# Kernel tuning notes

Measured on AMD Instinct MI355X. Metric: run time of the kernel, lower is better.

The kernel has to match this reference:

```python
import jax, jax.numpy as jnp
import numpy as np

B, N, F, T, O, K = 4, 4000, 16, 16, 16, 3
LN_EPS = 1e-5


def setup_inputs() -> dict:
    key = jax.random.key(0)
    k = jax.random.split(key, 18)
    rn = lambda i, sh, sc=1.0: jax.random.normal(k[i], sh, dtype=jnp.float32) * np.float32(sc)
    ru = lambda i, sh: jax.random.uniform(k[i], sh, dtype=jnp.float32)
    return {
        "x": rn(0, (B, N, F, T)),
        # scale the random Laplacian so the Chebyshev recurrence stays numerically sane
        "laplacian": rn(1, (N, N), 1.0 / np.sqrt(N)),
        "W1": ru(2, (T,)),
        "W2": rn(3, (F, T)),
        "W3": ru(4, (F,)),
        "bs": ru(5, (1, N, N)),
        "Vs": ru(6, (N, N)),
        "U1": ru(7, (N,)),
        "U2": rn(8, (F, N)),
        "U3": ru(9, (F,)),
        "be": ru(10, (1, T, T)),
        "Ve": ru(11, (T, T)),
        "cheb_w": rn(12, (K, F, O), 1.0 / np.sqrt(F)),
        "time_w": rn(13, (O, F, T), 1.0 / np.sqrt(F * T)),
        "time_b": rn(14, (O,)),
        "ln_g": jnp.ones((N, O), dtype=jnp.float32),
        "ln_b": jnp.zeros((N, O), dtype=jnp.float32),
    }


def reference(x, laplacian, W1, W2, W3, bs, Vs, U1, U2, U3, be, Ve,
              cheb_w, time_w, time_b, ln_g, ln_b):
    # ---- temporal attention: E (B,T,T) ----
    # lhs[b,t] = sum_{n,f} x[b,n,f,t] * U1[n]
    t_lhs = jnp.einsum('bnft,n->bt', x, U1)
    # rhs[b,t] = sum_{n,f,g} x[b,n,f,t] * U2[g,n] * U3[g]
    t_rhs = jnp.einsum('bnft,gn,g->bt', x, U2, U3)
    t_prod = t_lhs[:, :, None] * t_rhs[:, None, :]          # (B,T,T) outer product
    E = jnp.einsum('ts,bsr->btr', Ve, jax.nn.sigmoid(t_prod + be))
    E = jax.nn.softmax(E, axis=-1)

    # apply temporal attention along the time axis: (B,N,F,T)
    x_TAt = jnp.einsum('bts,bnfs->bnft', E, x)

    # ---- spatial attention: S (B,N,N) ----
    s_lhs = jnp.einsum('bnft,t->bnf', x, W1)                 # (B,N,F)
    # faithful to the source ops (valid since F == T here)
    s_rhs = jnp.einsum('bnkt,gk,t->bng', x, W2, W3)          # (B,N,F)
    s_prod = jnp.einsum('bnf,bmf->bnm', s_lhs, s_rhs)        # (B,N,N)
    S = jnp.einsum('nm,bmk->bnk', Vs, jax.nn.sigmoid(s_prod + bs))
    S = jax.nn.softmax(S, axis=-1)

    # spatially attended features for all timesteps at once
    x_SAtt = jnp.einsum('bnm,bmft->bnft', S, x_TAt)          # (B,N,F,T)

    # ---- Chebyshev graph conv over every timestep ----
    Tx0 = x_SAtt
    out = jnp.einsum('bnft,fo->bnot', Tx0, cheb_w[0])
    Tx1 = jnp.einsum('nm,bmft->bnft', laplacian, Tx0)
    out = out + jnp.einsum('bnft,fo->bnot', Tx1, cheb_w[1])
    for kk in range(2, K):
        Tx2 = 2.0 * jnp.einsum('nm,bmft->bnft', laplacian, Tx1) - Tx0
        out = out + jnp.einsum('bnft,fo->bnot', Tx2, cheb_w[kk])
        Tx0, Tx1 = Tx1, Tx2
    spatial_gcn_avg = out.mean(axis=-1)                      # (B,N,O)

    # ---- time conv: Conv2d(in,out,kernel=(1,T)) == full contraction over (F,T) ----
    time_out = jnp.einsum('bnct,oct->bno', x, time_w) + time_b

    # ---- residual (in_channels == out_channels branch) ----
    residual = x[:, :, :, -1]                                # (B,N,O)

    y = spatial_gcn_avg + time_out + residual
    # LayerNorm over the last two dims [N, O]
    mean = y.mean(axis=(1, 2), keepdims=True)
    var = jnp.var(y, axis=(1, 2), keepdims=True)
    y = (y - mean) / jnp.sqrt(var + LN_EPS) * ln_g + ln_b
    return jax.nn.relu(y)
```

## Files before the change

kernel.cpp:

```cpp
#include <hip/hip_runtime.h>
#include <math.h>

#define Bc 4
#define Nn 4000
#define KS 4096
#define NP (16000000 + 4096)

typedef _Float16 half8 __attribute__((ext_vector_type(8)));
typedef float f32x4 __attribute__((ext_vector_type(4)));
typedef unsigned short u16x4 __attribute__((ext_vector_type(4)));

static __device__ __forceinline__ unsigned short f2h(float f) {
  _Float16 h = (_Float16)f;
  unsigned short u;
  __builtin_memcpy(&u, &h, 2);
  return u;
}
static __device__ __forceinline__ float h2f(unsigned short u) {
  _Float16 h;
  __builtin_memcpy(&h, &u, 2);
  return (float)h;
}
static __device__ __forceinline__ void gld16(const void* g, void* l) {
  __builtin_amdgcn_global_load_lds(
      (const __attribute__((address_space(1))) unsigned int*)g,
      (__attribute__((address_space(3))) unsigned int*)l, 16, 0, 0);
}

__global__ __launch_bounds__(256) void k1_trhs(
    const float* __restrict__ x, const float* __restrict__ U1,
    const float* __restrict__ U2, const float* __restrict__ U3,
    float* __restrict__ tl, float* __restrict__ tr) {
  int b = blockIdx.y;
  int tid = threadIdx.x;
  int q = tid & 3;
  int n = blockIdx.x * 64 + (tid >> 2);
  float xs[16];
#pragma unroll
  for (int t = 0; t < 16; ++t) xs[t] = 0.f;
  float c1 = 0.f, c2 = 0.f;
  if (n < Nn) {
    const float* xr = x + ((size_t)b * Nn + n) * 256 + q * 64;
#pragma unroll
    for (int f = 0; f < 4; ++f) {
#pragma unroll
      for (int qq = 0; qq < 4; ++qq) {
        float4 v = *(const float4*)(xr + f * 16 + qq * 4);
        xs[qq * 4 + 0] += v.x; xs[qq * 4 + 1] += v.y;
        xs[qq * 4 + 2] += v.z; xs[qq * 4 + 3] += v.w;
      }
    }
    c1 = U1[n];
#pragma unroll
    for (int g = 0; g < 4; ++g) {
      int gg = q * 4 + g;
      c2 += U2[(size_t)gg * Nn + n] * U3[gg];
    }
  }
#pragma unroll
  for (int m = 1; m < 4; m <<= 1) {
    c2 += __shfl_xor(c2, m, 64);
#pragma unroll
    for (int t = 0; t < 16; ++t) xs[t] += __shfl_xor(xs[t], m, 64);
  }
  float v1[4], v2[4];
#pragma unroll
  for (int i = 0; i < 4; ++i) {
    int t = q * 4 + i;
    v1[i] = c1 * xs[t];
    v2[i] = c2 * xs[t];
  }
#pragma unroll
  for (int off = 4; off < 64; off <<= 1) {
#pragma unroll
    for (int i = 0; i < 4; ++i) {
      v1[i] += __shfl_down(v1[i], off, 64);
      v2[i] += __shfl_down(v2[i], off, 64);
    }
  }
  int lane = tid & 63;
  if (lane < 4) {
#pragma unroll
    for (int i = 0; i < 4; ++i) {
      atomicAdd(&tl[b * 16 + lane * 4 + i], v1[i]);
      atomicAdd(&tr[b * 16 + lane * 4 + i], v2[i]);
    }
  }
}

__global__ __launch_bounds__(256) void k2_eattn(
    const float* __restrict__ tl, const float* __restrict__ tr,
    const float* __restrict__ be, const float* __restrict__ Ve,
    float* __restrict__ ecol) {
  int b = blockIdx.x;
  int tid = threadIdx.x;
  __shared__ float sig[256];
  __shared__ float Em[256];
  int s = tid >> 4, r = tid & 15;
  float z = tl[b * 16 + s] * tr[b * 16 + r] + be[s * 16 + r];
  sig[s * 16 + r] = 1.0f / (1.0f + __expf(-z));
  __syncthreads();
  float e = 0.f;
#pragma unroll
  for (int ss = 0; ss < 16; ++ss) e += Ve[s * 16 + ss] * sig[ss * 16 + r];
  Em[s * 16 + r] = e;
  __syncthreads();
  if (tid < 16) {
    float m = -1e30f;
#pragma unroll
    for (int rr = 0; rr < 16; ++rr) m = fmaxf(m, Em[tid * 16 + rr]);
    float ssum = 0.f;
    float ex[16];
#pragma unroll
    for (int rr = 0; rr < 16; ++rr) { ex[rr] = __expf(Em[tid * 16 + rr] - m); ssum += ex[rr]; }
    float inv = 1.0f / ssum;
#pragma unroll
    for (int rr = 0; rr < 16; ++rr) Em[tid * 16 + rr] = ex[rr] * inv;
  }
  __syncthreads();
  if (tid < 16) {
    float c = 0.f;
#pragma unroll
    for (int tt = 0; tt < 16; ++tt) c += Em[tt * 16 + tid];
    ecol[b * 16 + tid] = c;
  }
}

__global__ __launch_bounds__(256) void k3_pern(
    const float* __restrict__ x, const float* __restrict__ ecol,
    const float* __restrict__ W1, const float* __restrict__ W2,
    const float* __restrict__ W3, const float* __restrict__ time_w,
    const float* __restrict__ time_b,
    float* __restrict__ xts, float* __restrict__ slhs,
    float* __restrict__ srhs, float* __restrict__ base) {
  __shared__ float tws[4096];
  __shared__ float W1s[16], W3s[16], Ecs[16], tbs[16], W2s[256];
  int tid = threadIdx.x;
  int b = blockIdx.y;
  for (int i = tid; i < 4096; i += 256) tws[i] = time_w[i];
  W2s[tid] = W2[tid & 255];
  if (tid < 16) {
    W1s[tid] = W1[tid]; W3s[tid] = W3[tid];
    Ecs[tid] = ecol[b * 16 + tid]; tbs[tid] = time_b[tid];
  }
  __syncthreads();
  int n = blockIdx.x * 256 + tid;
  if (n >= Nn) return;
  const float* xr = x + ((size_t)b * Nn + n) * 256;
  float xtsv[16], slv[16], xw3[16], to[16], resid[16];
#pragma unroll
  for (int i = 0; i < 16; ++i) { xtsv[i] = 0; slv[i] = 0; xw3[i] = 0; to[i] = 0; }
  for (int f = 0; f < 16; ++f) {
    float xf[16];
#pragma unroll
    for (int q = 0; q < 4; ++q) {
      float4 v = *(const float4*)(xr + f * 16 + q * 4);
      xf[q * 4 + 0] = v.x; xf[q * 4 + 1] = v.y; xf[q * 4 + 2] = v.z; xf[q * 4 + 3] = v.w;
    }
    float a = 0, c = 0, d = 0;
#pragma unroll
    for (int t2 = 0; t2 < 16; ++t2) {
      a += Ecs[t2] * xf[t2];
      c += W1s[t2] * xf[t2];
      d += W3s[t2] * xf[t2];
    }
    xtsv[f] = a; slv[f] = c; xw3[f] = d; resid[f] = xf[15];
#pragma unroll
    for (int o = 0; o < 16; ++o) {
      float acc = 0;
#pragma unroll
      for (int t2 = 0; t2 < 16; ++t2) acc += tws[o * 256 + f * 16 + t2] * xf[t2];
      to[o] += acc;
    }
  }
  size_t o16 = ((size_t)b * Nn + n) * 16;
#pragma unroll
  for (int g = 0; g < 16; ++g) {
    float acc = 0;
#pragma unroll
    for (int k2 = 0; k2 < 16; ++k2) acc += W2s[g * 16 + k2] * xw3[k2];
    srhs[o16 + g] = acc;
  }
#pragma unroll
  for (int i = 0; i < 16; ++i) {
    xts[o16 + i] = xtsv[i];
    slhs[o16 + i] = slv[i];
    base[o16 + i] = to[i] + tbs[i] + resid[i];
  }
}

__global__ __launch_bounds__(256) void fconv(
    const float* __restrict__ src, unsigned short* __restrict__ dst) {
  size_t i = ((size_t)blockIdx.x * 256 + threadIdx.x) * 4;
  float4 v = *(const float4*)(src + i);
  u16x4 h;
  h.x = f2h(v.x); h.y = f2h(v.y); h.z = f2h(v.z); h.w = f2h(v.w);
  *(u16x4*)(dst + i) = h;
}

__global__ __launch_bounds__(256) void vconv2(
    const float* __restrict__ Vs, unsigned short* __restrict__ Vh) {
  int row = blockIdx.y;
  int col = blockIdx.x * 1024 + threadIdx.x * 4;
  u16x4 h;
  if (row < Nn && col < Nn) {
    float4 v = *(const float4*)(Vs + (size_t)row * Nn + col);
    h.x = f2h(v.x); h.y = f2h(v.y); h.z = f2h(v.z); h.w = f2h(v.w);
  } else {
    h.x = 0; h.y = 0; h.z = 0; h.w = 0;
  }
  *(u16x4*)(Vh + (size_t)row * KS + col) = h;
}

__global__ __launch_bounds__(256) void tsconv(
    const float* __restrict__ ts, unsigned short* __restrict__ tsT) {
  int n = blockIdx.x * 256 + threadIdx.x;
  int col = blockIdx.y;
  if (n >= Nn) return;
  int b = col >> 4, f = col & 15;
  tsT[(size_t)col * Nn + n] = f2h(ts[((size_t)b * Nn + n) * 16 + f]);
}

__global__ __launch_bounds__(256) void gemm1_P(
    const float* __restrict__ slhs, const float* __restrict__ srhs,
    const unsigned short* __restrict__ bsH, unsigned short* __restrict__ PhT, int b) {
  __shared__ float Ms[64][17];
  __shared__ float Cs[64][17];
  __shared__ float Pt[64][65];
  int tid = threadIdx.x;
  int m0 = blockIdx.y * 64, k0 = blockIdx.x * 64;
  int lr = tid >> 2, lq = (tid & 3) << 2;
  {
    int gm = m0 + lr; if (gm > Nn - 1) gm = Nn - 1;
    float4 v = *(const float4*)(slhs + ((size_t)b * Nn + gm) * 16 + lq);
    Ms[lr][lq + 0] = v.x; Ms[lr][lq + 1] = v.y; Ms[lr][lq + 2] = v.z; Ms[lr][lq + 3] = v.w;
    int gk = k0 + lr; if (gk > Nn - 1) gk = Nn - 1;
    float4 w = *(const float4*)(srhs + ((size_t)b * Nn + gk) * 16 + lq);
    Cs[lr][lq + 0] = w.x; Cs[lr][lq + 1] = w.y; Cs[lr][lq + 2] = w.z; Cs[lr][lq + 3] = w.w;
  }
  __syncthreads();
  int tx = tid & 15, ty = tid >> 4;
  float acc[4][4] = {};
#pragma unroll
  for (int f = 0; f < 16; ++f) {
    float a4[4], b4[4];
#pragma unroll
    for (int i = 0; i < 4; ++i) a4[i] = Ms[ty * 4 + i][f];
#pragma unroll
    for (int j = 0; j < 4; ++j) b4[j] = Cs[tx * 4 + j][f];
#pragma unroll
    for (int i = 0; i < 4; ++i)
#pragma unroll
      for (int j = 0; j < 4; ++j) acc[i][j] += a4[i] * b4[j];
  }
#pragma unroll
  for (int i = 0; i < 4; ++i) {
    int m = m0 + ty * 4 + i;
    int k = k0 + tx * 4;
    float bv[4] = {0.f, 0.f, 0.f, 0.f};
    if (m < Nn) {
      if (k + 3 < Nn) {
        u16x4 t4 = *(const u16x4*)(bsH + (size_t)m * Nn + k);
        bv[0] = h2f(t4.x); bv[1] = h2f(t4.y); bv[2] = h2f(t4.z); bv[3] = h2f(t4.w);
      } else {
        for (int j = 0; j < 4; ++j)
          if (k + j < Nn) bv[j] = h2f(bsH[(size_t)m * Nn + k + j]);
      }
    }
#pragma unroll
    for (int j = 0; j < 4; ++j) {
      float z = acc[i][j] + bv[j];
      Pt[ty * 4 + i][tx * 4 + j] = 1.f / (1.f + __expf(-z));
    }
  }
  __syncthreads();
#pragma unroll
  for (int i = 0; i < 4; ++i) {
    int kl = ty * 4 + i;
    int ml = tx * 4;
    int gm = m0 + ml;
    u16x4 h;
    h.x = f2h(Pt[ml + 0][kl]);
    h.y = f2h(Pt[ml + 1][kl]);
    h.z = f2h(Pt[ml + 2][kl]);
    h.w = f2h(Pt[ml + 3][kl]);
    size_t off = (size_t)(k0 + kl) * KS + gm;
    if (gm + 3 < Nn) {
      *(u16x4*)(PhT + off) = h;
    } else {
      unsigned short hv[4] = {h.x, h.y, h.z, h.w};
      for (int q = 0; q < 4; ++q)
        if (gm + q < Nn) PhT[off + q] = hv[q];
    }
  }
}

__global__ __launch_bounds__(256) void gemm2_mfma(
    const unsigned short* __restrict__ Vh, const unsigned short* __restrict__ PhT,
    float* __restrict__ SP, unsigned int* __restrict__ rmaxu) {
  __shared__ unsigned short Ah[128 * 64];
  __shared__ unsigned short Bh[128 * 64];
  int t = threadIdx.x;
  int pid = blockIdx.x;
  int pm = (pid & 7) | ((pid >> 8) << 3);
  int pn = (pid >> 3) & 31;
  int row0 = pm * 128, col0 = pn * 128;

  int sr = t >> 3, ss = t & 7;
  int soct = ss ^ (sr & 7);
  size_t a_base = (size_t)(row0 + sr) * KS + soct * 8;
  size_t b_base = (size_t)(col0 + sr) * KS + soct * 8;

  int lane = t & 63;
  int wid = t >> 6;
  int wm = (wid >> 1) * 64, wn = (wid & 1) * 64;
  int ml = lane & 15, qd = lane >> 4;

  f32x4 acc[4][4] = {};

  for (int k0 = 0; k0 < KS; k0 += 64) {
#pragma unroll
    for (int p = 0; p < 4; ++p) {
      gld16(Vh + a_base + (size_t)(p * 32) * KS + k0, &Ah[p * 2048 + t * 8]);
      gld16(PhT + b_base + (size_t)(p * 32) * KS + k0, &Bh[p * 2048 + t * 8]);
    }
    __syncthreads();
#pragma unroll
    for (int kk = 0; kk < 2; ++kk) {
      half8 a_h[4], b_h[4];
#pragma unroll
      for (int i = 0; i < 4; ++i) {
        int r = wm + ml + i * 16;
        int slot = (kk * 4 + qd) ^ (r & 7);
        a_h[i] = *(const half8*)&Ah[r * 64 + slot * 8];
      }
#pragma unroll
      for (int j = 0; j < 4; ++j) {
        int r = wn + ml + j * 16;
        int slot = (kk * 4 + qd) ^ (r & 7);
        b_h[j] = *(const half8*)&Bh[r * 64 + slot * 8];
      }
#pragma unroll
      for (int i = 0; i < 4; ++i)
#pragma unroll
        for (int j = 0; j < 4; ++j)
          acc[i][j] = __builtin_amdgcn_mfma_f32_16x16x32_f16(a_h[i], b_h[j], acc[i][j], 0, 0, 0);
    }
    __syncthreads();
  }
#pragma unroll
  for (int i = 0; i < 4; ++i) {
#pragma unroll
    for (int r = 0; r < 4; ++r) {
      int grow = row0 + wm + i * 16 + qd * 4 + r;
      if (grow >= Nn) continue;
      float rowmax = -3.0e38f;
#pragma unroll
      for (int j = 0; j < 4; ++j) {
        int gcol = col0 + wn + j * 16 + ml;
        if (gcol < Nn) {
          float v = acc[i][j][r];
          SP[(size_t)grow * Nn + gcol] = v;
          rowmax = fmaxf(rowmax, v);
        }
      }
#pragma unroll
      for (int mk = 1; mk < 16; mk <<= 1)
        rowmax = fmaxf(rowmax, __shfl_xor(rowmax, mk, 64));
      if (ml == 0) {
        unsigned u = __float_as_uint(rowmax);
        u = (u & 0x80000000u) ? ~u : (u | 0x80000000u);
        atomicMax(rmaxu + grow, u);
      }
    }
  }
}

__global__ __launch_bounds__(256) void txsum_sp(
    const float* __restrict__ SP, const float* __restrict__ xts,
    const unsigned int* __restrict__ rmaxu, float* __restrict__ lsum,
    float* __restrict__ ts0, int b) {
  __shared__ float Ws[16][65];
  __shared__ float Xs[64][17];
  int tid = threadIdx.x;
  int n0 = blockIdx.x * 16;
  int kbase = blockIdx.y * 1000, kend = kbase + 1000;
  int r = tid >> 4, f = tid & 15;
  int lq = f * 4;
  int xr = tid >> 2, xc = (tid & 3) << 2;
  const float* spr = SP + (size_t)(n0 + r) * Nn;
  unsigned u = rmaxu[n0 + r];
  u = (u & 0x80000000u) ? (u ^ 0x80000000u) : ~u;
  float rm = __uint_as_float(u);
  float acc = 0.f, lpart = 0.f;
  for (int k0 = kbase; k0 < kend; k0 += 64) {
    int gx = k0 + xr;
    if (gx < kend) {
      float4 v = *(const float4*)(xts + ((size_t)b * Nn + gx) * 16 + xc);
      Xs[xr][xc + 0] = v.x; Xs[xr][xc + 1] = v.y; Xs[xr][xc + 2] = v.z; Xs[xr][xc + 3] = v.w;
    } else {
      Xs[xr][xc + 0] = 0.f; Xs[xr][xc + 1] = 0.f; Xs[xr][xc + 2] = 0.f; Xs[xr][xc + 3] = 0.f;
    }
    int gk = k0 + lq;
    float4 v = *(const float4*)(spr + gk);
    float e0 = (gk + 0 < kend) ? __expf(v.x - rm) : 0.f;
    float e1 = (gk + 1 < kend) ? __expf(v.y - rm) : 0.f;
    float e2 = (gk + 2 < kend) ? __expf(v.z - rm) : 0.f;
    float e3 = (gk + 3 < kend) ? __expf(v.w - rm) : 0.f;
    Ws[r][lq + 0] = e0; Ws[r][lq + 1] = e1; Ws[r][lq + 2] = e2; Ws[r][lq + 3] = e3;
    lpart += e0 + e1 + e2 + e3;
    __syncthreads();
#pragma unroll
    for (int kk = 0; kk < 64; ++kk) acc += Ws[r][kk] * Xs[kk][f];
    __syncthreads();
  }
#pragma unroll
  for (int mk = 1; mk < 16; mk <<= 1) lpart += __shfl_xor(lpart, mk, 64);
  if (f == 0) atomicAdd(&lsum[n0 + r], lpart);
  atomicAdd(&ts0[((size_t)b * Nn + n0 + r) * 16 + f], acc);
}

__global__ __launch_bounds__(256) void nrm_k(
    float* __restrict__ ts0, const float* __restrict__ lsum) {
  int tid = threadIdx.x;
  int b = blockIdx.y;
  int n = blockIdx.x * 16 + (tid >> 4);
  size_t i = ((size_t)b * Nn + n) * 16 + (tid & 15);
  ts0[i] = ts0[i] / lsum[b * Nn + n];
}

__global__ __launch_bounds__(256) void chebm(
    const unsigned short* __restrict__ lapH, const unsigned short* __restrict__ tsT,
    float* __restrict__ Cout) {
  __shared__ unsigned short Ah[64 * 32];
  __shared__ unsigned short Bh[64 * 32];
  int t = threadIdx.x;
  int row0 = blockIdx.x * 64;
  int kc0 = blockIdx.y * 25 * 32;
  int kc1 = kc0 + 25 * 32;
  int arow = row0 + (t >> 2); if (arow > Nn - 1) arow = Nn - 1;
  size_t a_base = (size_t)arow * Nn + (t & 3) * 8;
  size_t b_base = (size_t)(t >> 2) * Nn + (t & 3) * 8;

  int lane = t & 63;
  int wid = t >> 6;
  int wm = (wid >> 1) * 32, wn = (wid & 1) * 32;
  int ml = lane & 15, qd = lane >> 4;
  int aoff = (wm + ml) * 32 + qd * 8;
  int boff = (wn + ml) * 32 + qd * 8;

  f32x4 acc[2][2] = {};

  for (int k0 = kc0; k0 < kc1; k0 += 32) {
    gld16(lapH + a_base + k0, &Ah[t * 8]);
    gld16(tsT + b_base + k0, &Bh[t * 8]);
    __syncthreads();
    half8 a_h[2], b_h[2];
#pragma unroll
    for (int i = 0; i < 2; ++i) a_h[i] = *(const half8*)&Ah[aoff + i * 512];
#pragma unroll
    for (int j = 0; j < 2; ++j) b_h[j] = *(const half8*)&Bh[boff + j * 512];
#pragma unroll
    for (int i = 0; i < 2; ++i)
#pragma unroll
      for (int j = 0; j < 2; ++j)
        acc[i][j] = __builtin_amdgcn_mfma_f32_16x16x32_f16(a_h[i], b_h[j], acc[i][j], 0, 0, 0);
    __syncthreads();
  }
#pragma unroll
  for (int i = 0; i < 2; ++i)
#pragma unroll
    for (int j = 0; j < 2; ++j) {
      int gcol = wn + j * 16 + ml;
      int b = gcol >> 4, f = gcol & 15;
#pragma unroll
      for (int r = 0; r < 4; ++r) {
        int grow = row0 + wm + i * 16 + qd * 4 + r;
        if (grow < Nn) {
          size_t idx = ((size_t)b * Nn + grow) * 16 + f;
          atomicAdd(&Cout[idx], acc[i][j][r]);
        }
      }
    }
}

__global__ __launch_bounds__(256) void ky_k(
    const float* __restrict__ ts0, const float* __restrict__ ts1,
    const float* __restrict__ ts2, const float* __restrict__ cw,
    const float* __restrict__ base, float* __restrict__ ybuf,
    float* __restrict__ lnacc) {
  __shared__ float T0[256], T1[256], T2[256], CW[768];
  __shared__ float rs[256], rq[256];
  int tid = threadIdx.x;
  int b = blockIdx.y;
  size_t base_i = ((size_t)b * Nn + blockIdx.x * 16) * 16;
  T0[tid] = ts0[base_i + tid];
  T1[tid] = ts1[base_i + tid];
  T2[tid] = ts2[base_i + tid];
  for (int i = tid; i < 768; i += 256) CW[i] = cw[i];
  __syncthreads();
  int r = tid >> 4, o = tid & 15;
  float acc = 0.f;
#pragma unroll
  for (int f2 = 0; f2 < 16; ++f2) {
    float c2 = CW[512 + f2 * 16 + o];
    acc += T0[r * 16 + f2] * (CW[f2 * 16 + o] - c2);
    acc += T1[r * 16 + f2] * CW[256 + f2 * 16 + o];
    acc += (2.0f * T2[r * 16 + f2]) * c2;
  }
  float y = acc * 0.0625f + base[base_i + tid];
  ybuf[base_i + tid] = y;
  rs[tid] = y; rq[tid] = y * y;
  __syncthreads();
  for (int s2 = 128; s2 > 0; s2 >>= 1) {
    if (tid < s2) { rs[tid] += rs[tid + s2]; rq[tid] += rq[tid + s2]; }
    __syncthreads();
  }
  if (tid == 0) {
    atomicAdd(&lnacc[b * 2 + 0], rs[0]);
    atomicAdd(&lnacc[b * 2 + 1], rq[0]);
  }
}

__global__ __launch_bounds__(256) void kln_k(
    const float* __restrict__ ybuf, const float* __restrict__ lnacc,
    const float* __restrict__ lg, const float* __restrict__ lb,
    float* __restrict__ outp) {
  int tid = threadIdx.x;
  int b = blockIdx.y;
  size_t i = ((size_t)b * Nn + blockIdx.x * 16) * 16 + tid;
  size_t nz = (size_t)blockIdx.x * 256 + tid;
  const float inv = 1.0f / 64000.0f;
  float s = lnacc[b * 2 + 0], q = lnacc[b * 2 + 1];
  float mean = s * inv;
  float var = q * inv - mean * mean;
  float rstd = rsqrtf(var + 1e-5f);
  float v = (ybuf[i] - mean) * rstd * lg[nz] + lb[nz];
  outp[i] = fmaxf(v, 0.f);
}

extern "C" void kernel_launch(void* const* d_in, const int* in_sizes, int n_in,
                              void* d_out, int out_size, void* d_ws, size_t ws_size,
                              hipStream_t stream) {
  const float* x   = (const float*)d_in[0];
  const float* lap = (const float*)d_in[1];
  const float* W1  = (const float*)d_in[2];
  const float* W2  = (const float*)d_in[3];
  const float* W3  = (const float*)d_in[4];
  const float* bs  = (const float*)d_in[5];
  const float* Vs  = (const float*)d_in[6];
  const float* U1  = (const float*)d_in[7];
  const float* U2  = (const float*)d_in[8];
  const float* U3  = (const float*)d_in[9];
  const float* be  = (const float*)d_in[10];
  const float* Ve  = (const float*)d_in[11];
  const float* cw  = (const float*)d_in[12];
  const float* tw  = (const float*)d_in[13];
  const float* tb  = (const float*)d_in[14];
  const float* lg  = (const float*)d_in[15];
  const float* lb  = (const float*)d_in[16];
  float* ws = (float*)d_ws;
  float* SP = ws;
  unsigned short* Vh   = (unsigned short*)(ws + (size_t)NP);
  unsigned short* PhT  = Vh + (size_t)KS * KS;
  unsigned short* lapH = PhT + (size_t)KS * KS;
  unsigned short* bsH  = lapH + (size_t)Nn * Nn;
  unsigned short* tsT  = bsH + (size_t)Nn * Nn;
  float* xts  = (float*)(tsT + 64 * Nn + 64);
  float* slhs = xts + 256000;
  float* srhs = slhs + 256000;
  float* base = srhs + 256000;
  float* ts0  = base + 256000;
  float* ts1  = ts0 + 256000;
  float* ts2  = ts1 + 256000;
  float* ybuf = ts2 + 256000;
  float* tl   = ybuf + 256000;
  float* tr   = tl + 64;
  float* ecol = tr + 64;
  unsigned int* rmaxu = (unsigned int*)(ecol + 64);
  float* lsum = (float*)(rmaxu + Bc * Nn);
  float* lnacc = lsum + Bc * Nn;

  hipMemsetAsync(tl, 0, 128 * sizeof(float), stream);
  hipMemsetAsync(lnacc, 0, 8 * sizeof(float), stream);
  hipMemsetAsync(ts0, 0, 256000 * sizeof(float), stream);
  hipMemsetAsync(ts1, 0, 256000 * sizeof(float), stream);
  hipMemsetAsync(ts2, 0, 256000 * sizeof(float), stream);
  hipMemsetAsync(rmaxu, 0, Bc * Nn * sizeof(unsigned int), stream);
  hipMemsetAsync(lsum, 0, Bc * Nn * sizeof(float), stream);

  k1_trhs<<<dim3(63, 4), 256, 0, stream>>>(x, U1, U2, U3, tl, tr);
  k2_eattn<<<dim3(4), 256, 0, stream>>>(tl, tr, be, Ve, ecol);
  k3_pern<<<dim3(16, 4), 256, 0, stream>>>(x, ecol, W1, W2, W3, tw, tb,
                                           xts, slhs, srhs, base);
  vconv2<<<dim3(4, 4096), 256, 0, stream>>>(Vs, Vh);
  fconv<<<dim3(15625), 256, 0, stream>>>(lap, lapH);
  fconv<<<dim3(15625), 256, 0, stream>>>(bs, bsH);
  for (int b = 0; b < 4; ++b) {
    gemm1_P<<<dim3(63, 63), 256, 0, stream>>>(slhs, srhs, bsH, PhT, b);
    gemm2_mfma<<<dim3(1024), 256, 0, stream>>>(Vh, PhT, SP, rmaxu + b * Nn);
    txsum_sp<<<dim3(250, 4), 256, 0, stream>>>(SP, xts, rmaxu + b * Nn,
                                               lsum + b * Nn, ts0, b);
  }
  nrm_k<<<dim3(250, 4), 256, 0, stream>>>(ts0, lsum);
  tsconv<<<dim3(16, 64), 256, 0, stream>>>(ts0, tsT);
  chebm<<<dim3(63, 5), 256, 0, stream>>>(lapH, tsT, ts1);
  tsconv<<<dim3(16, 64), 256, 0, stream>>>(ts1, tsT);
  chebm<<<dim3(63, 5), 256, 0, stream>>>(lapH, tsT, ts2);
  ky_k<<<dim3(250, 4), 256, 0, stream>>>(ts0, ts1, ts2, cw, base, ybuf, lnacc);
  kln_k<<<dim3(250, 4), 256, 0, stream>>>(ybuf, lnacc, lg, lb, (float*)d_out);
}
```

Measured before the change: 1.320 ms.

## Rewrite Vs*P GEMM as 256x256-tile double-buffered pipelined MFMA kernel

Replaces the 128x128-tile, single-buffer gemm2 kernel with a 256x256 tile per 512-thread workgroup, using double-buffered LDS split into K halves and issuing async global-to-LDS loads for the next tiles during the MFMA phases. Explicit waitcnt, barriers and setprio interleave loading with compute, and the grid is remapped across 256 workgroups with an XCD-aware ordering. This aims to hide load latency and raise data reuse per tile. It needs more LDS and registers (8x4 accumulators), and 256 workgroups may underfill the GPU.

```diff
diff --git a/kernel.cpp b/kernel.cpp
--- a/kernel.cpp
+++ b/kernel.cpp
@@ -295,61 +295,118 @@
   }
 }
 
-__global__ __launch_bounds__(256) void gemm2_mfma(
+__global__ __launch_bounds__(512, 2) void gemm2_mfma(
     const unsigned short* __restrict__ Vh, const unsigned short* __restrict__ PhT,
     float* __restrict__ SP, unsigned int* __restrict__ rmaxu) {
-  __shared__ unsigned short Ah[128 * 64];
-  __shared__ unsigned short Bh[128 * 64];
+  __shared__ unsigned short Ah[2][2][8192];
+  __shared__ unsigned short Bh[2][2][8192];
   int t = threadIdx.x;
-  int pid = blockIdx.x;
-  int pm = (pid & 7) | ((pid >> 8) << 3);
-  int pn = (pid >> 3) & 31;
-  int row0 = pm * 128, col0 = pn * 128;
-
-  int sr = t >> 3, ss = t & 7;
-  int soct = ss ^ (sr & 7);
-  size_t a_base = (size_t)(row0 + sr) * KS + soct * 8;
-  size_t b_base = (size_t)(col0 + sr) * KS + soct * 8;
-
-  int lane = t & 63;
-  int wid = t >> 6;
-  int wm = (wid >> 1) * 64, wn = (wid & 1) * 64;
+  int bid = blockIdx.x;
+  int wg = (bid & 7) * 32 + (bid >> 3);
+  int row0 = (wg >> 4) * 256, col0 = (wg & 15) * 256;
+
+  int sr = t >> 2, sg = t & 3;
+  int ssw = sg ^ ((t >> 4) & 3);
+  size_t a0 = (size_t)(row0 + sr) * KS + ssw * 8;
+  size_t a1 = (size_t)(row0 + 128 + sr) * KS + ssw * 8;
+  size_t b0 = (size_t)(col0 + sr) * KS + ssw * 8;
+  size_t b1 = (size_t)(col0 + 128 + sr) * KS + ssw * 8;
+  int ld0 = t * 8, ld1 = 4096 + t * 8;
+
+  int lane = t & 63, wid = t >> 6;
+  int wm = (wid >> 2) * 128, wn = (wid & 3) * 64;
   int ml = lane & 15, qd = lane >> 4;
-
-  f32x4 acc[4][4] = {};
-
-  for (int k0 = 0; k0 < KS; k0 += 64) {
-#pragma unroll
-    for (int p = 0; p < 4; ++p) {
-      gld16(Vh + a_base + (size_t)(p * 32) * KS + k0, &Ah[p * 2048 + t * 8]);
-      gld16(PhT + b_base + (size_t)(p * 32) * KS + k0, &Bh[p * 2048 + t * 8]);
-    }
-    __syncthreads();
-#pragma unroll
-    for (int kk = 0; kk < 2; ++kk) {
-      half8 a_h[4], b_h[4];
-#pragma unroll
-      for (int i = 0; i < 4; ++i) {
-        int r = wm + ml + i * 16;
-        int slot = (kk * 4 + qd) ^ (r & 7);
-        a_h[i] = *(const half8*)&Ah[r * 64 + slot * 8];
-      }
-#pragma unroll
-      for (int j = 0; j < 4; ++j) {
-        int r = wn + ml + j * 16;
-        int slot = (kk * 4 + qd) ^ (r & 7);
-        b_h[j] = *(const half8*)&Bh[r * 64 + slot * 8];
-      }
-#pragma unroll
-      for (int i = 0; i < 4; ++i)
-#pragma unroll
-        for (int j = 0; j < 4; ++j)
-          acc[i][j] = __builtin_amdgcn_mfma_f32_16x16x32_f16(a_h[i], b_h[j], acc[i][j], 0, 0, 0);
-    }
-    __syncthreads();
-  }
-#pragma unroll
-  for (int i = 0; i < 4; ++i) {
+  int gr = qd ^ ((ml >> 2) & 3);
+  int aro[8], bro[4];
+#pragma unroll
+  for (int i = 0; i < 8; ++i) aro[i] = (wm + ml + i * 16) * 32 + gr * 8;
+#pragma unroll
+  for (int j = 0; j < 4; ++j) bro[j] = (wn + ml + j * 16) * 32 + gr * 8;
+
+  f32x4 acc[8][4] = {};
+
+#define STG(P, X, bf, kh, o0, o1, kt)                          \
+  do {                                                         \
+    size_t c_ = (size_t)(kt) * 64 + (kh) * 32;                 \
+    gld16(P + (o0) + c_, &X[bf][kh][ld0]);                     \
+    gld16(P + (o1) + c_, &X[bf][kh][ld1]);                     \
+  } while (0)
+
+  STG(Vh, Ah, 0, 0, a0, a1, 0); STG(PhT, Bh, 0, 0, b0, b1, 0);
+  STG(Vh, Ah, 0, 1, a0, a1, 0); STG(PhT, Bh, 0, 1, b0, b1, 0);
+  STG(Vh, Ah, 1, 0, a0, a1, 1); STG(PhT, Bh, 1, 0, b0, b1, 1);
+  STG(Vh, Ah, 1, 1, a0, a1, 1); STG(PhT, Bh, 1, 1, b0, b1, 1);
+  asm volatile("s_waitcnt vmcnt(12)" ::: "memory");
+  __builtin_amdgcn_s_barrier();
+
+#define PH_MFMA_BEGIN()                                        \
+  __builtin_amdgcn_s_barrier();                                \
+  asm volatile("s_waitcnt lgkmcnt(0)" ::: "memory");           \
+  __builtin_amdgcn_sched_barrier(0);                           \
+  __builtin_amdgcn_s_setprio(1)
+
+#pragma unroll 1
+  for (int G = 0; G < 64; ++G) {
+    int cb = G & 1, nb = cb ^ 1;
+    int tn1 = (G + 1 < 64) ? G + 1 : 63;
+    int tn2 = (G + 2 < 64) ? G + 2 : 63;
+    half8 av[4], bv[4];
+#pragma unroll
+    for (int j = 0; j < 4; ++j) bv[j] = *(const half8*)&Bh[cb][0][bro[j]];
+#pragma unroll
+    for (int i = 0; i < 4; ++i) av[i] = *(const half8*)&Ah[cb][0][aro[i]];
+    STG(Vh, Ah, nb, 1, a0, a1, tn1);
+    PH_MFMA_BEGIN();
+#pragma unroll
+    for (int i = 0; i < 4; ++i)
+#pragma unroll
+      for (int j = 0; j < 4; ++j)
+        acc[i][j] = __builtin_amdgcn_mfma_f32_16x16x32_f16(av[i], bv[j], acc[i][j], 0, 0, 0);
+    __builtin_amdgcn_s_setprio(0);
+    __builtin_amdgcn_s_barrier();
+#pragma unroll
+    for (int i = 0; i < 4; ++i) av[i] = *(const half8*)&Ah[cb][0][aro[4 + i]];
+    STG(PhT, Bh, nb, 1, b0, b1, tn1);
+    PH_MFMA_BEGIN();
+#pragma unroll
+    for (int i = 0; i < 4; ++i)
+#pragma unroll
+      for (int j = 0; j < 4; ++j)
+        acc[4 + i][j] = __builtin_amdgcn_mfma_f32_16x16x32_f16(av[i], bv[j], acc[4 + i][j], 0, 0, 0);
+    __builtin_amdgcn_s_setprio(0);
+    asm volatile("s_waitcnt vmcnt(8)" ::: "memory");
+    __builtin_amdgcn_s_barrier();
+#pragma unroll
+    for (int j = 0; j < 4; ++j) bv[j] = *(const half8*)&Bh[cb][1][bro[j]];
+#pragma unroll
+    for (int i = 0; i < 4; ++i) av[i] = *(const half8*)&Ah[cb][1][aro[i]];
+    STG(Vh, Ah, cb, 0, a0, a1, tn2);
+    PH_MFMA_BEGIN();
+#pragma unroll
+    for (int i = 0; i < 4; ++i)
+#pragma unroll
+      for (int j = 0; j < 4; ++j)
+        acc[i][j] = __builtin_amdgcn_mfma_f32_16x16x32_f16(av[i], bv[j], acc[i][j], 0, 0, 0);
+    __builtin_amdgcn_s_setprio(0);
+    __builtin_amdgcn_s_barrier();
+#pragma unroll
+    for (int i = 0; i < 4; ++i) av[i] = *(const half8*)&Ah[cb][1][aro[4 + i]];
+    STG(PhT, Bh, cb, 0, b0, b1, tn2);
+    PH_MFMA_BEGIN();
+#pragma unroll
+    for (int i = 0; i < 4; ++i)
+#pragma unroll
+      for (int j = 0; j < 4; ++j)
+        acc[4 + i][j] = __builtin_amdgcn_mfma_f32_16x16x32_f16(av[i], bv[j], acc[4 + i][j], 0, 0, 0);
+    __builtin_amdgcn_s_setprio(0);
+    asm volatile("s_waitcnt vmcnt(8)" ::: "memory");
+    __builtin_amdgcn_s_barrier();
+  }
+#undef STG
+#undef PH_MFMA_BEGIN
+
+#pragma unroll
+  for (int i = 0; i < 8; ++i) {
 #pragma unroll
     for (int r = 0; r < 4; ++r) {
       int grow = row0 + wm + i * 16 + qd * 4 + r;
@@ -598,7 +655,7 @@
   fconv<<<dim3(15625), 256, 0, stream>>>(bs, bsH);
   for (int b = 0; b < 4; ++b) {
     gemm1_P<<<dim3(63, 63), 256, 0, stream>>>(slhs, srhs, bsH, PhT, b);
-    gemm2_mfma<<<dim3(1024), 256, 0, stream>>>(Vh, PhT, SP, rmaxu + b * Nn);
+    gemm2_mfma<<<dim3(256), 512, 0, stream>>>(Vh, PhT, SP, rmaxu + b * Nn);
     txsum_sp<<<dim3(250, 4), 256, 0, stream>>>(SP, xts, rmaxu + b * Nn,
                                                lsum + b * Nn, ts0, b);
   }
```

After: 1.252 ms. 5.1% less time.
